# Performance work log

Hardware: AMD Instinct MI355X
Metric: run time of the kernel (lower is better)

## Reference

```python
import jax, jax.numpy as jnp
import numpy as np
from jax import lax

GAMMA = 0.99
TAU = 0.95
B = 4194304  # batchsz (flat trajectory length)


def setup_inputs() -> dict:
    key = jax.random.key(0)
    k_r, k_v, k_m = jax.random.split(key, 3)
    r = jax.random.normal(k_r, (B,), dtype=jnp.float32)
    v = jax.random.normal(k_v, (B,), dtype=jnp.float32)
    mask = jax.random.randint(k_m, (B,), 0, 2, dtype=jnp.int32)  # 0 = episode end
    return {"r": r, "v": v, "mask": mask}


def reference(r, v, mask):
    """GAE advantage + V-target via a reverse linear-recurrence scan.

    v_target[t] = r[t] + gamma * v_target[t+1] * mask[t]
    delta[t]    = r[t] + gamma * v[t+1]        * mask[t] - v[t]
    A_sa[t]     = delta[t] + gamma * tau * A_sa[t+1] * mask[t]
    A_sa normalized to zero mean / unit (unbiased) std, as in torch .std().
    """
    m = mask.astype(r.dtype)

    def step(carry, x):
        prev_vt, prev_v, prev_A = carry
        r_t, v_t, m_t = x
        vt = r_t + GAMMA * prev_vt * m_t
        delta = r_t + GAMMA * prev_v * m_t - v_t
        A = delta + GAMMA * TAU * prev_A * m_t
        return (vt, v_t, A), (vt, A)

    zero = jnp.float32(0.0)
    _, (v_target, A_sa) = lax.scan(step, (zero, zero, zero), (r, v, m), reverse=True)
    A_sa = (A_sa - A_sa.mean()) / jnp.std(A_sa, ddof=1)
    return A_sa, v_target
```

## Files before the change

### kernel.cpp

```cpp
#include <hip/hip_runtime.h>
#include <math.h>

#define BTOT 4194304
#define TPB  256
#define EPT  16
#define CS   (TPB * EPT)
#define NCH  (BTOT / CS)
#define CPT  (NCH / TPB)


__constant__ const float kG  = 0.99f;
__constant__ const float kGT = 0.99f * 0.95f;

__device__ __forceinline__ float wave_redf(float x) {
#pragma unroll
    for (int o = 32; o > 0; o >>= 1) x += __shfl_down(x, o);
    return x;
}
__device__ __forceinline__ double wave_redd(double x) {
#pragma unroll
    for (int o = 32; o > 0; o >>= 1) x += __shfl_down(x, o);
    return x;
}

__device__ __forceinline__ void block_suffix_scan(
    float pv, float sv, float pa, float sa,
    float* lpv, float* lsv, float* lpa, float* lsa, int j)
{
    lpv[j] = pv; lsv[j] = sv; lpa[j] = pa; lsa[j] = sa;
    __syncthreads();
#pragma unroll
    for (int d = 1; d < TPB; d <<= 1) {
        float cpv = lpv[j], csv = lsv[j], cpa = lpa[j], csa = lsa[j];
        bool has = (j + d) < TPB;
        float qpv = 1.0f, qsv = 0.0f, qpa = 1.0f, qsa = 0.0f;
        if (has) { qpv = lpv[j+d]; qsv = lsv[j+d]; qpa = lpa[j+d]; qsa = lsa[j+d]; }
        __syncthreads();
        if (has) {
            lpv[j] = cpv * qpv; lsv[j] = csv + cpv * qsv;
            lpa[j] = cpa * qpa; lsa[j] = csa + cpa * qsa;
        }
        __syncthreads();
    }
}

__global__ __launch_bounds__(TPB) void ppo_k1_summarize(
    const float* __restrict__ r, const float* __restrict__ v,
    const int* __restrict__ mk, float* __restrict__ ws) {
    const int c = blockIdx.x;
    const int j = threadIdx.x;
    const int base = c * CS + j * EPT;

    float rr[EPT], vv[EPT + 1], dd[EPT];
    int mm[EPT];
    const float4* r4 = (const float4*)(r + base);
    const float4* v4 = (const float4*)(v + base);
    const int4*   m4 = (const int4*)(mk + base);
#pragma unroll
    for (int k = 0; k < EPT / 4; ++k) {
        float4 a = r4[k];
        rr[4*k] = a.x; rr[4*k+1] = a.y; rr[4*k+2] = a.z; rr[4*k+3] = a.w;
        float4 b = v4[k];
        vv[4*k] = b.x; vv[4*k+1] = b.y; vv[4*k+2] = b.z; vv[4*k+3] = b.w;
        int4 m = m4[k];
        mm[4*k] = m.x; mm[4*k+1] = m.y; mm[4*k+2] = m.z; mm[4*k+3] = m.w;
    }
    vv[EPT] = (base + EPT < BTOT) ? v[base + EPT] : 0.0f;

#pragma unroll
    for (int k = 0; k < EPT; ++k) {
        float m = (float)mm[k];
        dd[k] = rr[k] + kG * m * vv[k + 1] - vv[k];
    }

    float pv = 1.0f, sv = 0.0f, pa = 1.0f, sa = 0.0f;
#pragma unroll
    for (int k = EPT - 1; k >= 0; --k) {
        float m = (float)mm[k];
        float av = kG * m, aa = kGT * m;
        sv = rr[k] + av * sv;
        sa = dd[k] + aa * sa;
        pv *= av; pa *= aa;
    }

    __shared__ float lpv[TPB], lsv[TPB], lpa[TPB], lsa[TPB];
    block_suffix_scan(pv, sv, pa, sa, lpv, lsv, lpa, lsa, j);

    float CinA = (j + 1 < TPB) ? lsa[j + 1] : 0.0f;
    float QrA  = (j + 1 < TPB) ? lpa[j + 1] : 1.0f;
    float chPv = lpv[0], chSv = lsv[0], chPa = lpa[0], chSa = lsa[0];

    float x = CinA, ql = 1.0f;
    float s0 = 0, s1 = 0, s2 = 0, s3 = 0, s4 = 0;
#pragma unroll
    for (int k = EPT - 1; k >= 0; --k) {
        float m = (float)mm[k];
        float aa = kGT * m;
        x = dd[k] + aa * x;
        ql *= aa;
        float q = ql * QrA;
        s0 += x; s1 += q; s2 += x * x; s3 += x * q; s4 += q * q;
    }
    s0 = wave_redf(s0); s1 = wave_redf(s1); s2 = wave_redf(s2);
    s3 = wave_redf(s3); s4 = wave_redf(s4);
    __shared__ float rb[4][5];
    int wid = j >> 6, ln = j & 63;
    if (ln == 0) { rb[wid][0]=s0; rb[wid][1]=s1; rb[wid][2]=s2; rb[wid][3]=s3; rb[wid][4]=s4; }
    __syncthreads();
    if (j == 0) {
        float t0=0,t1=0,t2=0,t3=0,t4=0;
        for (int w = 0; w < 4; ++w) { t0+=rb[w][0]; t1+=rb[w][1]; t2+=rb[w][2]; t3+=rb[w][3]; t4+=rb[w][4]; }
        ws[0*NCH+c] = chPv; ws[1*NCH+c] = chSv; ws[2*NCH+c] = chPa; ws[3*NCH+c] = chSa;
        ws[4*NCH+c] = t0;   ws[5*NCH+c] = t1;   ws[6*NCH+c] = t2;
        ws[7*NCH+c] = t3;   ws[8*NCH+c] = t4;
    }
}

__global__ __launch_bounds__(TPB) void ppo_k2_finalize(
    const float* __restrict__ r, const float* __restrict__ v,
    const int* __restrict__ mk, const float* __restrict__ ws,
    float* __restrict__ outA, float* __restrict__ outV)
{
    const int c = blockIdx.x;
    const int j = threadIdx.x;
    const int base = c * CS + j * EPT;

    __shared__ float lpv[TPB], lsv[TPB], lpa[TPB], lsa[TPB];
    __shared__ double rd[4][2];
    __shared__ float bcast[4];

    {
        float cpv[CPT], csv[CPT], cpa[CPT], csa[CPT];
        {
            float4 t;
            t = *(const float4*)(ws + 0*NCH + 4*j); cpv[0]=t.x; cpv[1]=t.y; cpv[2]=t.z; cpv[3]=t.w;
            t = *(const float4*)(ws + 1*NCH + 4*j); csv[0]=t.x; csv[1]=t.y; csv[2]=t.z; csv[3]=t.w;
            t = *(const float4*)(ws + 2*NCH + 4*j); cpa[0]=t.x; cpa[1]=t.y; cpa[2]=t.z; cpa[3]=t.w;
            t = *(const float4*)(ws + 3*NCH + 4*j); csa[0]=t.x; csa[1]=t.y; csa[2]=t.z; csa[3]=t.w;
        }
        float gpv = 1.0f, gsv = 0.0f, gpa = 1.0f, gsa = 0.0f;
#pragma unroll
        for (int i = CPT - 1; i >= 0; --i) {
            gsv = csv[i] + cpv[i] * gsv; gpv = cpv[i] * gpv;
            gsa = csa[i] + cpa[i] * gsa; gpa = cpa[i] * gpa;
        }

        block_suffix_scan(gpv, gsv, gpa, gsa, lpv, lsv, lpa, lsa, j);

        float Cv = (j + 1 < TPB) ? lsv[j + 1] : 0.0f;
        float Ca = (j + 1 < TPB) ? lsa[j + 1] : 0.0f;

        float sLv[CPT], sqv[CPT], sL2v[CPT], sLqv[CPT], sq2v[CPT];
        {
            float4 t;
            t = *(const float4*)(ws + 4*NCH + 4*j); sLv[0]=t.x;  sLv[1]=t.y;  sLv[2]=t.z;  sLv[3]=t.w;
            t = *(const float4*)(ws + 5*NCH + 4*j); sqv[0]=t.x;  sqv[1]=t.y;  sqv[2]=t.z;  sqv[3]=t.w;
            t = *(const float4*)(ws + 6*NCH + 4*j); sL2v[0]=t.x; sL2v[1]=t.y; sL2v[2]=t.z; sL2v[3]=t.w;
            t = *(const float4*)(ws + 7*NCH + 4*j); sLqv[0]=t.x; sLqv[1]=t.y; sLqv[2]=t.z; sLqv[3]=t.w;
            t = *(const float4*)(ws + 8*NCH + 4*j); sq2v[0]=t.x; sq2v[1]=t.y; sq2v[2]=t.z; sq2v[3]=t.w;
        }
        double dS = 0.0, dS2 = 0.0;
#pragma unroll
        for (int i = CPT - 1; i >= 0; --i) {
            int g = 4*j + i;
            if (g == c) { bcast[0] = Cv; bcast[1] = Ca; }
            dS  += (double)(sLv[i]  + Ca * sqv[i]);
            dS2 += (double)(sL2v[i] + 2.0f * Ca * sLqv[i] + Ca * Ca * sq2v[i]);
            Cv = csv[i] + cpv[i] * Cv;
            Ca = csa[i] + cpa[i] * Ca;
        }
        dS = wave_redd(dS); dS2 = wave_redd(dS2);
        int wid = j >> 6, ln = j & 63;
        if (ln == 0) { rd[wid][0] = dS; rd[wid][1] = dS2; }
        __syncthreads();
        if (j == 0) {
            double S  = rd[0][0] + rd[1][0] + rd[2][0] + rd[3][0];
            double S2 = rd[0][1] + rd[1][1] + rd[2][1] + rd[3][1];
            double n = (double)BTOT;
            double mean = S / n;
            double var = (S2 - S * mean) / (n - 1.0);
            bcast[2] = (float)mean;
            bcast[3] = (float)(1.0 / sqrt(var));
        }
        __syncthreads();
    }

    float rr[EPT], vv[EPT + 1], dd[EPT];
    int mm[EPT];
    const float4* r4 = (const float4*)(r + base);
    const float4* v4 = (const float4*)(v + base);
    const int4*   m4 = (const int4*)(mk + base);
#pragma unroll
    for (int k = 0; k < EPT / 4; ++k) {
        float4 a = r4[k];
        rr[4*k] = a.x; rr[4*k+1] = a.y; rr[4*k+2] = a.z; rr[4*k+3] = a.w;
        float4 b = v4[k];
        vv[4*k] = b.x; vv[4*k+1] = b.y; vv[4*k+2] = b.z; vv[4*k+3] = b.w;
        int4 m = m4[k];
        mm[4*k] = m.x; mm[4*k+1] = m.y; mm[4*k+2] = m.z; mm[4*k+3] = m.w;
    }
    vv[EPT] = (base + EPT < BTOT) ? v[base + EPT] : 0.0f;
#pragma unroll
    for (int k = 0; k < EPT; ++k) {
        float m = (float)mm[k];
        dd[k] = rr[k] + kG * m * vv[k + 1] - vv[k];
    }

    float pv = 1.0f, sv = 0.0f, pa = 1.0f, sa = 0.0f;
#pragma unroll
    for (int k = EPT - 1; k >= 0; --k) {
        float m = (float)mm[k];
        float av = kG * m, aa = kGT * m;
        sv = rr[k] + av * sv;
        sa = dd[k] + aa * sa;
        pv *= av; pa *= aa;
    }
    block_suffix_scan(pv, sv, pa, sa, lpv, lsv, lpa, lsa, j);

    float CinV = (j + 1 < TPB) ? lsv[j + 1] : 0.0f;
    float QrV  = (j + 1 < TPB) ? lpv[j + 1] : 1.0f;
    float CinA = (j + 1 < TPB) ? lsa[j + 1] : 0.0f;
    float QrA  = (j + 1 < TPB) ? lpa[j + 1] : 1.0f;

    const float Ccv  = bcast[0];
    const float Cca  = bcast[1];
    const float mean = bcast[2];
    const float inv  = bcast[3];

    float xv = CinV + QrV * Ccv;
    float xa = CinA + QrA * Cca;
    float oA[EPT], oV[EPT];
#pragma unroll
    for (int k = EPT - 1; k >= 0; --k) {
        float m = (float)mm[k];
        xv = rr[k] + kG  * m * xv;
        xa = dd[k] + kGT * m * xa;
        oV[k] = xv;
        oA[k] = (xa - mean) * inv;
    }
    float4* a4 = (float4*)(outA + base);
    float4* w4 = (float4*)(outV + base);
#pragma unroll
    for (int k = 0; k < EPT / 4; ++k) {
        a4[k] = make_float4(oA[4*k], oA[4*k+1], oA[4*k+2], oA[4*k+3]);
        w4[k] = make_float4(oV[4*k], oV[4*k+1], oV[4*k+2], oV[4*k+3]);
    }
}

extern "C" void kernel_launch(void* const* d_in, const int* in_sizes, int n_in,
                              void* d_out, int out_size, void* d_ws, size_t ws_size,
                              hipStream_t stream) {
    const float* r  = (const float*)d_in[0];
    const float* v  = (const float*)d_in[1];
    const int*   mk = (const int*)d_in[2];
    float* outA = (float*)d_out;
    float* outV = outA + BTOT;
    float* ws   = (float*)d_ws;

    hipLaunchKernelGGL(ppo_k1_summarize, dim3(NCH), dim3(TPB), 0, stream,
                       r, v, mk, ws);
    hipLaunchKernelGGL(ppo_k2_finalize, dim3(NCH), dim3(TPB), 0, stream,
                       r, v, mk, ws, outA, outV);
}
```

Baseline: 116.2 us.

## Fuse summarize and finalize passes into one cooperative kernel with grid sync

Replaces the two-kernel scheme with a single cooperative kernel that keeps r, delta and mask bits in registers across a grid-wide barrier. This removes the second read of the inputs from global memory and one kernel launch. It needs all 1024 blocks to be co-resident (4 blocks per CU requested) and falls back to the old two-kernel path if the cooperative launch fails. Grid sync overhead and register pressure from holding data across the barrier are the trade-off.

```diff
diff --git a/kernel.cpp b/kernel.cpp
--- a/kernel.cpp
+++ b/kernel.cpp
@@ -1,5 +1,8 @@
 #include <hip/hip_runtime.h>
+#include <hip/hip_cooperative_groups.h>
 #include <math.h>
+
+namespace cg = cooperative_groups;
 
 #define BTOT 4194304
 #define TPB  256
@@ -41,6 +44,173 @@
             lpa[j] = cpa * qpa; lsa[j] = csa + cpa * qsa;
         }
         __syncthreads();
+    }
+}
+
+__global__ __launch_bounds__(TPB, 4) void ppo_fused(
+    const float* __restrict__ r, const float* __restrict__ v,
+    const int* __restrict__ mk, float* __restrict__ ws,
+    float* __restrict__ outA, float* __restrict__ outV)
+{
+    const int c = blockIdx.x;
+    const int j = threadIdx.x;
+    const int base = c * CS + j * EPT;
+
+    __shared__ float lpv[TPB], lsv[TPB], lpa[TPB], lsa[TPB];
+    __shared__ float rb[4][5];
+    __shared__ double rd[4][2];
+    __shared__ float bcast[4];
+
+    float rr[EPT], dd[EPT];
+    unsigned mb = 0;
+    {
+        float vv[EPT + 1];
+        int mm[EPT];
+        const float4* r4 = (const float4*)(r + base);
+        const float4* v4 = (const float4*)(v + base);
+        const int4*   m4 = (const int4*)(mk + base);
+#pragma unroll
+        for (int k = 0; k < EPT / 4; ++k) {
+            float4 a = r4[k];
+            rr[4*k] = a.x; rr[4*k+1] = a.y; rr[4*k+2] = a.z; rr[4*k+3] = a.w;
+            float4 b = v4[k];
+            vv[4*k] = b.x; vv[4*k+1] = b.y; vv[4*k+2] = b.z; vv[4*k+3] = b.w;
+            int4 m = m4[k];
+            mm[4*k] = m.x; mm[4*k+1] = m.y; mm[4*k+2] = m.z; mm[4*k+3] = m.w;
+        }
+        vv[EPT] = (base + EPT < BTOT) ? v[base + EPT] : 0.0f;
+#pragma unroll
+        for (int k = 0; k < EPT; ++k) {
+            mb |= ((unsigned)(mm[k] & 1)) << k;
+            float m = (float)mm[k];
+            dd[k] = rr[k] + kG * m * vv[k + 1] - vv[k];
+        }
+    }
+
+    float pv = 1.0f, sv = 0.0f, pa = 1.0f, sa = 0.0f;
+#pragma unroll
+    for (int k = EPT - 1; k >= 0; --k) {
+        float m = (float)((mb >> k) & 1u);
+        float av = kG * m, aa = kGT * m;
+        sv = rr[k] + av * sv;
+        sa = dd[k] + aa * sa;
+        pv *= av; pa *= aa;
+    }
+    block_suffix_scan(pv, sv, pa, sa, lpv, lsv, lpa, lsa, j);
+
+    float CinV = (j + 1 < TPB) ? lsv[j + 1] : 0.0f;
+    float QrV  = (j + 1 < TPB) ? lpv[j + 1] : 1.0f;
+    float CinA = (j + 1 < TPB) ? lsa[j + 1] : 0.0f;
+    float QrA  = (j + 1 < TPB) ? lpa[j + 1] : 1.0f;
+
+    {
+        float x = CinA, ql = 1.0f;
+        float s0 = 0, s1 = 0, s2 = 0, s3 = 0, s4 = 0;
+#pragma unroll
+        for (int k = EPT - 1; k >= 0; --k) {
+            float m = (float)((mb >> k) & 1u);
+            float aa = kGT * m;
+            x = dd[k] + aa * x;
+            ql *= aa;
+            float q = ql * QrA;
+            s0 += x; s1 += q; s2 += x * x; s3 += x * q; s4 += q * q;
+        }
+        s0 = wave_redf(s0); s1 = wave_redf(s1); s2 = wave_redf(s2);
+        s3 = wave_redf(s3); s4 = wave_redf(s4);
+        int wid = j >> 6, ln = j & 63;
+        if (ln == 0) { rb[wid][0]=s0; rb[wid][1]=s1; rb[wid][2]=s2; rb[wid][3]=s3; rb[wid][4]=s4; }
+        __syncthreads();
+        if (j == 0) {
+            float t0=0,t1=0,t2=0,t3=0,t4=0;
+            for (int w = 0; w < 4; ++w) { t0+=rb[w][0]; t1+=rb[w][1]; t2+=rb[w][2]; t3+=rb[w][3]; t4+=rb[w][4]; }
+            ws[0*NCH+c] = lpv[0]; ws[1*NCH+c] = lsv[0];
+            ws[2*NCH+c] = lpa[0]; ws[3*NCH+c] = lsa[0];
+            ws[4*NCH+c] = t0;     ws[5*NCH+c] = t1;     ws[6*NCH+c] = t2;
+            ws[7*NCH+c] = t3;     ws[8*NCH+c] = t4;
+            __threadfence();
+        }
+    }
+
+    cg::this_grid().sync();
+
+    float Ccv, Cca, mean, inv;
+    {
+        float cpv[CPT], csv[CPT], cpa[CPT], csa[CPT];
+        {
+            float4 t;
+            t = *(const float4*)(ws + 0*NCH + 4*j); cpv[0]=t.x; cpv[1]=t.y; cpv[2]=t.z; cpv[3]=t.w;
+            t = *(const float4*)(ws + 1*NCH + 4*j); csv[0]=t.x; csv[1]=t.y; csv[2]=t.z; csv[3]=t.w;
+            t = *(const float4*)(ws + 2*NCH + 4*j); cpa[0]=t.x; cpa[1]=t.y; cpa[2]=t.z; cpa[3]=t.w;
+            t = *(const float4*)(ws + 3*NCH + 4*j); csa[0]=t.x; csa[1]=t.y; csa[2]=t.z; csa[3]=t.w;
+        }
+        float gpv = 1.0f, gsv = 0.0f, gpa = 1.0f, gsa = 0.0f;
+#pragma unroll
+        for (int i = CPT - 1; i >= 0; --i) {
+            gsv = csv[i] + cpv[i] * gsv; gpv = cpv[i] * gpv;
+            gsa = csa[i] + cpa[i] * gsa; gpa = cpa[i] * gpa;
+        }
+
+        block_suffix_scan(gpv, gsv, gpa, gsa, lpv, lsv, lpa, lsa, j);
+
+        float Cv = (j + 1 < TPB) ? lsv[j + 1] : 0.0f;
+        float Ca = (j + 1 < TPB) ? lsa[j + 1] : 0.0f;
+
+        float sLv[CPT], sqv[CPT], sL2v[CPT], sLqv[CPT], sq2v[CPT];
+        {
+            float4 t;
+            t = *(const float4*)(ws + 4*NCH + 4*j); sLv[0]=t.x;  sLv[1]=t.y;  sLv[2]=t.z;  sLv[3]=t.w;
+            t = *(const float4*)(ws + 5*NCH + 4*j); sqv[0]=t.x;  sqv[1]=t.y;  sqv[2]=t.z;  sqv[3]=t.w;
+            t = *(const float4*)(ws + 6*NCH + 4*j); sL2v[0]=t.x; sL2v[1]=t.y; sL2v[2]=t.z; sL2v[3]=t.w;
+            t = *(const float4*)(ws + 7*NCH + 4*j); sLqv[0]=t.x; sLqv[1]=t.y; sLqv[2]=t.z; sLqv[3]=t.w;
+            t = *(const float4*)(ws + 8*NCH + 4*j); sq2v[0]=t.x; sq2v[1]=t.y; sq2v[2]=t.z; sq2v[3]=t.w;
+        }
+        double dS = 0.0, dS2 = 0.0;
+#pragma unroll
+        for (int i = CPT - 1; i >= 0; --i) {
+            int g = 4*j + i;
+            if (g == c) { bcast[0] = Cv; bcast[1] = Ca; }
+            dS  += (double)(sLv[i]  + Ca * sqv[i]);
+            dS2 += (double)(sL2v[i] + 2.0f * Ca * sLqv[i] + Ca * Ca * sq2v[i]);
+            Cv = csv[i] + cpv[i] * Cv;
+            Ca = csa[i] + cpa[i] * Ca;
+        }
+        dS = wave_redd(dS); dS2 = wave_redd(dS2);
+        int wid = j >> 6, ln = j & 63;
+        if (ln == 0) { rd[wid][0] = dS; rd[wid][1] = dS2; }
+        __syncthreads();
+        if (j == 0) {
+            double S  = rd[0][0] + rd[1][0] + rd[2][0] + rd[3][0];
+            double S2 = rd[0][1] + rd[1][1] + rd[2][1] + rd[3][1];
+            double n = (double)BTOT;
+            double m_ = S / n;
+            double var = (S2 - S * m_) / (n - 1.0);
+            bcast[2] = (float)m_;
+            bcast[3] = (float)(1.0 / sqrt(var));
+        }
+        __syncthreads();
+        Ccv  = bcast[0];
+        Cca  = bcast[1];
+        mean = bcast[2];
+        inv  = bcast[3];
+    }
+
+    float xv = CinV + QrV * Ccv;
+    float xa = CinA + QrA * Cca;
+    float oA[EPT], oV[EPT];
+#pragma unroll
+    for (int k = EPT - 1; k >= 0; --k) {
+        float m = (float)((mb >> k) & 1u);
+        xv = rr[k] + kG  * m * xv;
+        xa = dd[k] + kGT * m * xa;
+        oV[k] = xv;
+        oA[k] = (xa - mean) * inv;
+    }
+    float4* a4 = (float4*)(outA + base);
+    float4* w4 = (float4*)(outV + base);
+#pragma unroll
+    for (int k = 0; k < EPT / 4; ++k) {
+        a4[k] = make_float4(oA[4*k], oA[4*k+1], oA[4*k+2], oA[4*k+3]);
+        w4[k] = make_float4(oV[4*k], oV[4*k+1], oV[4*k+2], oV[4*k+3]);
     }
 }
 
@@ -257,8 +427,16 @@
     float* outV = outA + BTOT;
     float* ws   = (float*)d_ws;
 
-    hipLaunchKernelGGL(ppo_k1_summarize, dim3(NCH), dim3(TPB), 0, stream,
-                       r, v, mk, ws);
-    hipLaunchKernelGGL(ppo_k2_finalize, dim3(NCH), dim3(TPB), 0, stream,
-                       r, v, mk, ws, outA, outV);
-}
+    void* args[6];
+    args[0] = (void*)&r;    args[1] = (void*)&v;    args[2] = (void*)&mk;
+    args[3] = (void*)&ws;   args[4] = (void*)&outA; args[5] = (void*)&outV;
+
+    hipError_t e = hipLaunchCooperativeKernel(
+        (const void*)ppo_fused, dim3(NCH), dim3(TPB), args, 0, stream);
+    if (e != hipSuccess) {
+        hipLaunchKernelGGL(ppo_k1_summarize, dim3(NCH), dim3(TPB), 0, stream,
+                           r, v, mk, ws);
+        hipLaunchKernelGGL(ppo_k2_finalize, dim3(NCH), dim3(TPB), 0, stream,
+                           r, v, mk, ws, outA, outV);
+    }
+}
```

New measurement: 237.9 us. +104.8%, slower.

## Cache delta, packed mask bits and carries in workspace for the finalize pass

Applied to the files above, without the earlier changes.

The summarize kernel now writes the per-element delta values, a 16-bit packed mask word per thread, and per-thread carry-in values for both recurrences to the workspace. The finalize kernel reads these instead of re-reading v and mask, and it drops the recomputation of delta and the block suffix scan. This removes redundant arithmetic and a shared-memory scan with its barriers from the second pass. In exchange it adds roughly 21 MB of workspace writes and reads, so total memory traffic grows slightly. It also assumes the workspace is large enough for these buffers and that mask values are exactly 0 or 1.

```diff
diff --git a/kernel.cpp b/kernel.cpp
--- a/kernel.cpp
+++ b/kernel.cpp
@@ -8,6 +8,10 @@
 #define NCH  (BTOT / CS)
 #define CPT  (NCH / TPB)
 
+#define WS_SUM 0
+#define WS_DD  16384
+#define WS_MB  (WS_DD + BTOT)
+#define WS_CAR (WS_MB + BTOT / 16)
 
 __constant__ const float kG  = 0.99f;
 __constant__ const float kGT = 0.99f * 0.95f;
@@ -67,10 +71,20 @@
     }
     vv[EPT] = (base + EPT < BTOT) ? v[base + EPT] : 0.0f;
 
+    unsigned mb = 0;
 #pragma unroll
     for (int k = 0; k < EPT; ++k) {
+        mb |= ((unsigned)(mm[k] & 1)) << k;
         float m = (float)mm[k];
         dd[k] = rr[k] + kG * m * vv[k + 1] - vv[k];
+    }
+
+    {
+        float4* d4 = (float4*)(ws + WS_DD + base);
+#pragma unroll
+        for (int k = 0; k < EPT / 4; ++k)
+            d4[k] = make_float4(dd[4*k], dd[4*k+1], dd[4*k+2], dd[4*k+3]);
+        ((unsigned*)(ws + WS_MB))[c * TPB + j] = mb;
     }
 
     float pv = 1.0f, sv = 0.0f, pa = 1.0f, sa = 0.0f;
@@ -86,9 +100,14 @@
     __shared__ float lpv[TPB], lsv[TPB], lpa[TPB], lsa[TPB];
     block_suffix_scan(pv, sv, pa, sa, lpv, lsv, lpa, lsa, j);
 
+    float CinV = (j + 1 < TPB) ? lsv[j + 1] : 0.0f;
+    float QrV  = (j + 1 < TPB) ? lpv[j + 1] : 1.0f;
     float CinA = (j + 1 < TPB) ? lsa[j + 1] : 0.0f;
     float QrA  = (j + 1 < TPB) ? lpa[j + 1] : 1.0f;
     float chPv = lpv[0], chSv = lsv[0], chPa = lpa[0], chSa = lsa[0];
+
+    *(float4*)(ws + WS_CAR + 4 * (c * TPB + j)) =
+        make_float4(CinV, QrV, CinA, QrA);
 
     float x = CinA, ql = 1.0f;
     float s0 = 0, s1 = 0, s2 = 0, s3 = 0, s4 = 0;
@@ -117,8 +136,7 @@
 }
 
 __global__ __launch_bounds__(TPB) void ppo_k2_finalize(
-    const float* __restrict__ r, const float* __restrict__ v,
-    const int* __restrict__ mk, const float* __restrict__ ws,
+    const float* __restrict__ r, const float* __restrict__ ws,
     float* __restrict__ outA, float* __restrict__ outV)
 {
     const int c = blockIdx.x;
@@ -185,54 +203,32 @@
         __syncthreads();
     }
 
-    float rr[EPT], vv[EPT + 1], dd[EPT];
-    int mm[EPT];
-    const float4* r4 = (const float4*)(r + base);
-    const float4* v4 = (const float4*)(v + base);
-    const int4*   m4 = (const int4*)(mk + base);
-#pragma unroll
-    for (int k = 0; k < EPT / 4; ++k) {
-        float4 a = r4[k];
-        rr[4*k] = a.x; rr[4*k+1] = a.y; rr[4*k+2] = a.z; rr[4*k+3] = a.w;
-        float4 b = v4[k];
-        vv[4*k] = b.x; vv[4*k+1] = b.y; vv[4*k+2] = b.z; vv[4*k+3] = b.w;
-        int4 m = m4[k];
-        mm[4*k] = m.x; mm[4*k+1] = m.y; mm[4*k+2] = m.z; mm[4*k+3] = m.w;
-    }
-    vv[EPT] = (base + EPT < BTOT) ? v[base + EPT] : 0.0f;
-#pragma unroll
-    for (int k = 0; k < EPT; ++k) {
-        float m = (float)mm[k];
-        dd[k] = rr[k] + kG * m * vv[k + 1] - vv[k];
-    }
-
-    float pv = 1.0f, sv = 0.0f, pa = 1.0f, sa = 0.0f;
-#pragma unroll
-    for (int k = EPT - 1; k >= 0; --k) {
-        float m = (float)mm[k];
-        float av = kG * m, aa = kGT * m;
-        sv = rr[k] + av * sv;
-        sa = dd[k] + aa * sa;
-        pv *= av; pa *= aa;
-    }
-    block_suffix_scan(pv, sv, pa, sa, lpv, lsv, lpa, lsa, j);
-
-    float CinV = (j + 1 < TPB) ? lsv[j + 1] : 0.0f;
-    float QrV  = (j + 1 < TPB) ? lpv[j + 1] : 1.0f;
-    float CinA = (j + 1 < TPB) ? lsa[j + 1] : 0.0f;
-    float QrA  = (j + 1 < TPB) ? lpa[j + 1] : 1.0f;
+    float rr[EPT], dd[EPT];
+    {
+        const float4* r4 = (const float4*)(r + base);
+        const float4* d4 = (const float4*)(ws + WS_DD + base);
+#pragma unroll
+        for (int k = 0; k < EPT / 4; ++k) {
+            float4 a = r4[k];
+            rr[4*k] = a.x; rr[4*k+1] = a.y; rr[4*k+2] = a.z; rr[4*k+3] = a.w;
+            float4 b = d4[k];
+            dd[4*k] = b.x; dd[4*k+1] = b.y; dd[4*k+2] = b.z; dd[4*k+3] = b.w;
+        }
+    }
+    const unsigned mb = ((const unsigned*)(ws + WS_MB))[c * TPB + j];
+    const float4 car = *(const float4*)(ws + WS_CAR + 4 * (c * TPB + j));
 
     const float Ccv  = bcast[0];
     const float Cca  = bcast[1];
     const float mean = bcast[2];
     const float inv  = bcast[3];
 
-    float xv = CinV + QrV * Ccv;
-    float xa = CinA + QrA * Cca;
+    float xv = car.x + car.y * Ccv;
+    float xa = car.z + car.w * Cca;
     float oA[EPT], oV[EPT];
 #pragma unroll
     for (int k = EPT - 1; k >= 0; --k) {
-        float m = (float)mm[k];
+        float m = (float)((mb >> k) & 1u);
         xv = rr[k] + kG  * m * xv;
         xa = dd[k] + kGT * m * xa;
         oV[k] = xv;
@@ -260,5 +256,5 @@
     hipLaunchKernelGGL(ppo_k1_summarize, dim3(NCH), dim3(TPB), 0, stream,
                        r, v, mk, ws);
     hipLaunchKernelGGL(ppo_k2_finalize, dim3(NCH), dim3(TPB), 0, stream,
-                       r, v, mk, ws, outA, outV);
-}
+                       r, ws, outA, outV);
+}
```

Result: slower. 119.9 us (+3.3%).
